# Kernel optimization log

Hardware: AMD Instinct MI355X
Metric: run time of the kernel (lower is better)

## Reference

```python
import jax, jax.numpy as jnp
import numpy as np

IN_F, OUT_F, NB = 4096, 4096, 8
BS = IN_F // NB  # 512


def setup_inputs() -> dict:
    key = jax.random.key(0)
    k1, k2, k3, k4 = jax.random.split(key, 4)
    weight = jax.random.normal(k1, (OUT_F, IN_F), dtype=jnp.float32) * 0.02
    bias = jax.random.normal(k2, (OUT_F,), dtype=jnp.float32) * 0.02
    x = jax.random.normal(k3, (4, 2048, IN_F), dtype=jnp.float32)
    R_blocks = jax.random.normal(k4, (NB, BS, BS), dtype=jnp.float32) * 0.1
    return {"weight": weight, "bias": bias, "x": x, "R_blocks": R_blocks, "layer_idx": 0}


def cayley_transform(A):
    # A: [nb, bs, bs]; Q = (I - A_skew) @ inv(I + A_skew + 1e-6 I)
    bs = A.shape[-1]
    I = jnp.eye(bs, dtype=A.dtype)
    A_skew = 0.5 * (A - jnp.swapaxes(A, -2, -1))
    return jnp.matmul(I - A_skew, jnp.linalg.inv(I + A_skew + 1e-6 * I))


def reference(weight, bias, x, R_blocks, layer_idx):
    R_ortho = cayley_transform(R_blocks)  # [nb, bs, bs]
    # weight @ block_diag(R) == per-block contraction on the in_features axis
    w = weight.reshape(OUT_F, NB, BS)
    tw = jnp.einsum('onb,nbc->onc', w, R_ortho).reshape(OUT_F, IN_F)
    # F.linear: x @ tw.T + bias
    out = jnp.einsum('bsi,oi->bso', x, tw) + bias
    return out
```

## Files before the change

### kernel.cpp

```cpp
#include <hip/hip_runtime.h>
#include <hip/hip_bf16.h>


typedef unsigned short u16;
typedef __attribute__((ext_vector_type(8))) __bf16 bf16x8;
typedef __attribute__((ext_vector_type(4))) float f32x4;
typedef __attribute__((ext_vector_type(8))) unsigned short u16x8;
typedef __attribute__((ext_vector_type(4))) unsigned short u16x4;

#define C0   1.000001f
#define C1Q  2.000001f
#define AS1 __attribute__((address_space(1)))
#define AS3 __attribute__((address_space(3)))

__device__ __forceinline__ u16 f2bf(float x) {
  union { float f; unsigned u; } v; v.f = x;
  return (u16)((v.u + 0x7fffu + ((v.u >> 16) & 1u)) >> 16);
}
__device__ __forceinline__ float bf2f(u16 h) {
  union { float f; unsigned u; } v; v.u = ((unsigned)h) << 16; return v.f;
}

__global__ __launch_bounds__(256) void k_build_M(const float* __restrict__ R,
                                                 u16* __restrict__ Mh,
                                                 u16* __restrict__ Ml) {
  __shared__ float t1[32][33];
  const int n = blockIdx.z;
  const int tr = blockIdx.y * 32, tc = blockIdx.x * 32;
  const int ly = threadIdx.x >> 5, lx = threadIdx.x & 31;
  const float* Rb = R + (size_t)n * 262144;
  float a[4];
#pragma unroll
  for (int i = 0; i < 4; ++i) {
    a[i] = Rb[(size_t)(tr + ly + i * 8) * 512 + tc + lx];
    t1[ly + i * 8][lx] = Rb[(size_t)(tc + ly + i * 8) * 512 + tr + lx];
  }
  __syncthreads();
#pragma unroll
  for (int i = 0; i < 4; ++i) {
    const int r = tr + ly + i * 8, c = tc + lx;
    float m = 0.5f * (a[i] - t1[lx][ly + i * 8]) + (r == c ? C0 : 0.0f);
    u16 h = f2bf(m);
    const size_t idx = (size_t)n * 262144 + (size_t)r * 512 + c;
    Mh[idx] = h;
    Ml[idx] = f2bf(m - bf2f(h));
  }
}

__global__ __launch_bounds__(1024) void k_frob_alpha(const u16* __restrict__ G4,
                                                     float* __restrict__ alpha) {
  __shared__ float red[16];
  const int n = blockIdx.x, tid = threadIdx.x;
  const u16* src = G4 + (size_t)n * 262144;
  float s = 0.f;
  for (int i = tid; i < 32768; i += 1024) {
    u16x8 v = reinterpret_cast<const u16x8*>(src)[i];
#pragma unroll
    for (int e = 0; e < 8; ++e) { float f = bf2f(v[e]); s += f * f; }
  }
  for (int off = 32; off; off >>= 1) s += __shfl_down(s, off, 64);
  if ((tid & 63) == 0) red[tid >> 6] = s;
  __syncthreads();
  if (tid == 0) {
    float t = 0.f;
    for (int q = 0; q < 16; ++q) t += red[q];
    float lam = powf(t, 0.125f);
    alpha[n] = 2.0f / (C0 * C0 + lam);
  }
}

__global__ __launch_bounds__(256) void k_init_X0(const u16* __restrict__ Mh,
                                                 const u16* __restrict__ Ml,
                                                 const float* __restrict__ alpha,
                                                 u16* __restrict__ X0,
                                                 u16* __restrict__ X0t) {
  int idx = blockIdx.x * 256 + threadIdx.x;
  int n = idx >> 18, r = (idx >> 9) & 511, c = idx & 511;
  float m = bf2f(Mh[idx]) + bf2f(Ml[idx]);
  float a = alpha[n];
  X0[idx]  = f2bf(a * ((r == c ? 2.0f * C0 : 0.0f) - m));
  X0t[idx] = f2bf(a * m);
}

template <int PROD3, int DMODE, int OMODE>
__global__ __launch_bounds__(256)
void k_bmm(const u16* __restrict__ Ah, const u16* __restrict__ Al,
           const u16* __restrict__ Bh, const u16* __restrict__ Bl,
           const u16* __restrict__ Dh, const u16* __restrict__ Dl,
           u16* __restrict__ Cnh, u16* __restrict__ Cnl,
           u16* __restrict__ Cth, u16* __restrict__ Ctl,
           float* __restrict__ Cf, float cd, float cs) {
  __shared__ __align__(16) u16 sAh[2048], sBh[2048];
  __shared__ __align__(16) u16 sAl[PROD3 ? 2048 : 8], sBl[PROD3 ? 2048 : 8];
  const size_t zb = (size_t)blockIdx.z * 262144;
  const int tid = threadIdx.x, lane = tid & 63, wave = tid >> 6;
  const int m0 = blockIdx.y * 64, n0 = blockIdx.x * 64;
  const int wr = wave >> 1, wc = wave & 1;
  const int c15 = lane & 15, lk = lane >> 4;
  const int srow = tid >> 2;
  const int sg = (tid & 3) ^ (srow & 3);
  f32x4 acc[2][2] = {};
  const u16* pa = Ah + zb + (size_t)(m0 + srow) * 512 + sg * 8;
  const u16* pb = Bh + zb + (size_t)(n0 + srow) * 512 + sg * 8;

  for (int k0 = 0; k0 < 512; k0 += 32) {
    __builtin_amdgcn_global_load_lds((const AS1 void*)(pa + k0),
                                     (AS3 void*)(sAh + (size_t)tid * 8), 16, 0, 0);
    __builtin_amdgcn_global_load_lds((const AS1 void*)(pb + k0),
                                     (AS3 void*)(sBh + (size_t)tid * 8), 16, 0, 0);
    if constexpr (PROD3) {
      const u16* pal = Al + zb + (size_t)(m0 + srow) * 512 + sg * 8;
      const u16* pbl = Bl + zb + (size_t)(n0 + srow) * 512 + sg * 8;
      __builtin_amdgcn_global_load_lds((const AS1 void*)(pal + k0),
                                       (AS3 void*)(sAl + (size_t)tid * 8), 16, 0, 0);
      __builtin_amdgcn_global_load_lds((const AS1 void*)(pbl + k0),
                                       (AS3 void*)(sBl + (size_t)tid * 8), 16, 0, 0);
    }
    __syncthreads();
    bf16x8 a[2], b[2], al2[2], bl2[2];
#pragma unroll
    for (int i = 0; i < 2; ++i) {
      const int fr = wr * 32 + i * 16 + c15;
      const int ia = fr * 32 + ((lk ^ (fr & 3)) * 8);
      a[i] = *reinterpret_cast<const bf16x8*>(&sAh[ia]);
      if constexpr (PROD3) al2[i] = *reinterpret_cast<const bf16x8*>(&sAl[ia]);
    }
#pragma unroll
    for (int j = 0; j < 2; ++j) {
      const int fc = wc * 32 + j * 16 + c15;
      const int ib = fc * 32 + ((lk ^ (fc & 3)) * 8);
      b[j] = *reinterpret_cast<const bf16x8*>(&sBh[ib]);
      if constexpr (PROD3) bl2[j] = *reinterpret_cast<const bf16x8*>(&sBl[ib]);
    }
#pragma unroll
    for (int i = 0; i < 2; ++i)
#pragma unroll
      for (int j = 0; j < 2; ++j) {
        acc[i][j] = __builtin_amdgcn_mfma_f32_16x16x32_bf16(a[i], b[j], acc[i][j], 0, 0, 0);
        if constexpr (PROD3) {
          acc[i][j] = __builtin_amdgcn_mfma_f32_16x16x32_bf16(a[i],   bl2[j], acc[i][j], 0, 0, 0);
          acc[i][j] = __builtin_amdgcn_mfma_f32_16x16x32_bf16(al2[i], b[j],   acc[i][j], 0, 0, 0);
        }
      }
    __syncthreads();
  }
#pragma unroll
  for (int i = 0; i < 2; ++i)
#pragma unroll
    for (int j = 0; j < 2; ++j) {
      const int rowb = m0 + wr * 32 + i * 16 + lk * 4;
      const int col  = n0 + wc * 32 + j * 16 + c15;
      u16 hv[4], lv[4];
#pragma unroll
      for (int r = 0; r < 4; ++r) {
        float val = cs * acc[i][j][r];
        if constexpr (DMODE >= 1) {
          float d = bf2f(Dh[zb + (size_t)(rowb + r) * 512 + col]);
          if constexpr (DMODE == 2) d += bf2f(Dl[zb + (size_t)(rowb + r) * 512 + col]);
          val += cd * d;
        }
        if constexpr (OMODE & 16) Cf[zb + (size_t)(rowb + r) * 512 + col] = val;
        u16 h = f2bf(val);
        if constexpr (OMODE & 1) Cnh[zb + (size_t)(rowb + r) * 512 + col] = h;
        u16 l = 0;
        if constexpr (OMODE & 10) l = f2bf(val - bf2f(h));
        if constexpr (OMODE & 2) Cnl[zb + (size_t)(rowb + r) * 512 + col] = l;
        hv[r] = h; lv[r] = l;
      }
      if constexpr (OMODE & 4) {
        u16x4 v; v[0] = hv[0]; v[1] = hv[1]; v[2] = hv[2]; v[3] = hv[3];
        *reinterpret_cast<u16x4*>(&Cth[zb + (size_t)col * 512 + rowb]) = v;
      }
      if constexpr (OMODE & 8) {
        u16x4 v; v[0] = lv[0]; v[1] = lv[1]; v[2] = lv[2]; v[3] = lv[3];
        *reinterpret_cast<u16x4*>(&Ctl[zb + (size_t)col * 512 + rowb]) = v;
      }
    }
}

template <int SPLIT, int BF16OUT>
__global__ __launch_bounds__(256)
void k_smm(const float* __restrict__ A, int lda, long long astride,
           const float* __restrict__ B, int ldb, long long bstride,
           void* __restrict__ Cv, int ldc, long long cstride,
           const float* __restrict__ D, int ldd, long long dstride,
           float c1, float sgn, int K) {
  __shared__ __align__(16) u16 lA  [128 * 40];
  __shared__ __align__(16) u16 lBT [128 * 40];
  const int nz = blockIdx.z;
  const float* Ab = A + (size_t)nz * astride;
  const float* Bb = B + (size_t)nz * bstride;
  const float* Db = D + (size_t)nz * dstride;
  const int tid = threadIdx.x, lane = tid & 63, wave = tid >> 6;
  const int m0 = blockIdx.y * 128, n0 = blockIdx.x * 128;
  const int wr = wave >> 1, wc = wave & 1;
  f32x4 acc[4][4] = {};

  for (int k0 = 0; k0 < K; k0 += 32) {
    if (k0) __syncthreads();
    {
      const int row = tid >> 1, ks = (tid & 1) * 16;
      const float* src = Ab + (size_t)(m0 + row) * lda + k0 + ks;
      float fv[16];
#pragma unroll
      for (int q = 0; q < 4; ++q) {
        float4 f = *(reinterpret_cast<const float4*>(src) + q);
        fv[q * 4 + 0] = f.x; fv[q * 4 + 1] = f.y; fv[q * 4 + 2] = f.z; fv[q * 4 + 3] = f.w;
      }
      u16x8 w0, w1;
#pragma unroll
      for (int e = 0; e < 8; ++e) { w0[e] = f2bf(fv[e]); w1[e] = f2bf(fv[e + 8]); }
      *reinterpret_cast<u16x8*>(&lA[row * 40 + ks])     = w0;
      *reinterpret_cast<u16x8*>(&lA[row * 40 + ks + 8]) = w1;
    }
    {
      const int kk = tid >> 3, nb = (tid & 7) * 16;
      const float* src = Bb + (size_t)(k0 + kk) * ldb + n0 + nb;
      float fv[16];
#pragma unroll
      for (int q = 0; q < 4; ++q) {
        float4 f = *(reinterpret_cast<const float4*>(src) + q);
        fv[q * 4 + 0] = f.x; fv[q * 4 + 1] = f.y; fv[q * 4 + 2] = f.z; fv[q * 4 + 3] = f.w;
      }
#pragma unroll
      for (int e = 0; e < 16; ++e) lBT[(nb + e) * 40 + kk] = f2bf(fv[e]);
    }
    __syncthreads();
    const int ks = (lane >> 4) * 8;
    bf16x8 af[4], bfr[4];
#pragma unroll
    for (int f = 0; f < 4; ++f) {
      const int ar = wr * 64 + f * 16 + (lane & 15);
      const int bc = wc * 64 + f * 16 + (lane & 15);
      af[f]  = *reinterpret_cast<const bf16x8*>(&lA [ar * 40 + ks]);
      bfr[f] = *reinterpret_cast<const bf16x8*>(&lBT[bc * 40 + ks]);
    }
#pragma unroll
    for (int i = 0; i < 4; ++i)
#pragma unroll
      for (int j = 0; j < 4; ++j)
        acc[i][j] = __builtin_amdgcn_mfma_f32_16x16x32_bf16(af[i], bfr[j], acc[i][j], 0, 0, 0);
  }
#pragma unroll
  for (int i = 0; i < 4; ++i) {
    const int rowb = m0 + wr * 64 + i * 16 + ((lane >> 4) << 2);
#pragma unroll
    for (int j = 0; j < 4; ++j) {
      const int col = n0 + wc * 64 + j * 16 + (lane & 15);
#pragma unroll
      for (int r = 0; r < 4; ++r) {
        float val = sgn * acc[i][j][r];
        if (c1 != 0.0f) val += c1 * Db[(size_t)(rowb + r) * ldd + col];
        if constexpr (BF16OUT)
          reinterpret_cast<u16*>(Cv)[(size_t)nz * cstride + (size_t)(rowb + r) * ldc + col] = f2bf(val);
        else
          reinterpret_cast<float*>(Cv)[(size_t)nz * cstride + (size_t)(rowb + r) * ldc + col] = val;
      }
    }
  }
}

__global__ __launch_bounds__(256) void k_f32_to_bf16(const float* __restrict__ in,
                                                     u16* __restrict__ out) {
  int idx = blockIdx.x * 256 + threadIdx.x;
  const float* src = in + (size_t)idx * 8;
  float4 f0 = *reinterpret_cast<const float4*>(src);
  float4 f1 = *reinterpret_cast<const float4*>(src + 4);
  u16x8 w;
  w[0] = f2bf(f0.x); w[1] = f2bf(f0.y); w[2] = f2bf(f0.z); w[3] = f2bf(f0.w);
  w[4] = f2bf(f1.x); w[5] = f2bf(f1.y); w[6] = f2bf(f1.z); w[7] = f2bf(f1.w);
  *reinterpret_cast<u16x8*>(out + (size_t)idx * 8) = w;
}

#define NSL 18

#define RD_A3(dst, MH)                                                         \
  _Pragma("unroll")                                                            \
  for (int m = 0; m < 4; ++m)                                                  \
    dst[m] = *reinterpret_cast<const bf16x8*>(                                 \
        &lds[aslot * 4096 + ((MH) * 64 + m * 16 + c15) * 32 + gsw * 8]);

#define RD_B3(dst)                                                             \
  _Pragma("unroll")                                                            \
  for (int n = 0; n < 4; ++n)                                                  \
    dst[n] = *reinterpret_cast<const bf16x8*>(                                 \
        &lds[bslot * 4096 + (bq64 + n * 16 + c15) * 32 + gsw * 8]);

#define MFMA16(afX, bfX, MH)                                                   \
  __builtin_amdgcn_s_setprio(1);                                               \
  _Pragma("unroll")                                                            \
  for (int m = 0; m < 4; ++m)                                                  \
    _Pragma("unroll")                                                          \
    for (int n = 0; n < 4; ++n)                                                \
      acc[(MH) * 4 + m][n] = __builtin_amdgcn_mfma_f32_16x16x32_bf16(          \
          afX[m], bfX[n], acc[(MH) * 4 + m][n], 0, 0, 0);                      \
  __builtin_amdgcn_s_setprio(0);

#define TILE32(WM)                                                             \
  {                                                                            \
    int aslot = s0 + wr;            if (aslot >= NSL) aslot -= NSL;            \
    int bslot = s0 + 2 + (wc >> 1); if (bslot >= NSL) bslot -= NSL;            \
    STAGE(); STAGE();                                                          \
    RD_B3(bfr)                                                                 \
    RD_A3(afA, 0)                                                              \
    MFMA16(afA, bfr, 0)                                                        \
    STAGE(); STAGE();                                                          \
    RD_A3(afB, 1)                                                              \
    MFMA16(afB, bfr, 1)                                                        \
    if ((WM) == 1) asm volatile("s_waitcnt vmcnt(8)" ::: "memory");            \
    if ((WM) == 2) asm volatile("s_waitcnt vmcnt(4)" ::: "memory");            \
    if ((WM) == 3) asm volatile("s_waitcnt vmcnt(0)" ::: "memory");            \
    if ((WM) != 0) {                                                           \
      __builtin_amdgcn_s_barrier();                                            \
      __builtin_amdgcn_sched_barrier(0);                                       \
    }                                                                          \
    s0 += 4; if (s0 >= NSL) s0 -= NSL;                                         \
  }

__global__ __launch_bounds__(512, 2)
void k_gemm256(const u16* __restrict__ A, const u16* __restrict__ B,
               const float* __restrict__ bias,
               float* __restrict__ C, int N, int K) {
  __shared__ __align__(16) u16 lds[NSL * 4096];
  const int tid = threadIdx.x, lane = tid & 63, wave = tid >> 6;
  int bid = blockIdx.y * gridDim.x + blockIdx.x;
  const int cpx = (gridDim.x * gridDim.y) >> 3;
  bid = (bid & 7) * cpx + (bid >> 3);
  const int nbx = N >> 8;
  const int bx = bid % nbx, by = bid / nbx;
  const int m0 = by << 8, n0 = bx << 8;
  const int wr = wave >> 2, wc = wave & 3;
  const int srow = tid >> 2;
  const int sgc  = (tid & 3) ^ ((srow >> 1) & 3);
  const int c15 = lane & 15, lq = lane >> 4;
  const int gsw = lq ^ ((c15 >> 1) & 3);
  const int bq64 = (wc & 1) * 64;
  const int NT = K >> 5;

  f32x4 acc[8][4] = {};
  bf16x8 afA[4], afB[4], bfr[4];

  int jn = 0, js = 0;
  auto STAGE = [&]() {
    if (jn < 4 * NT) {
      const int t = jn >> 2, q = jn & 3;
      const u16* srcb = (q < 2)
          ? A + (size_t)(m0 + q * 128 + srow) * (size_t)K
          : B + (size_t)(n0 + (q - 2) * 128 + srow) * (size_t)K;
      const u16* src = srcb + (t << 5) + sgc * 8;
      u16* dst = (u16*)lds + js * 4096 + tid * 8;
      __builtin_amdgcn_global_load_lds(
          (const AS1 void*)src, (AS3 void*)dst, 16, 0, 0);
    }
    ++jn; js = (js == NSL - 1) ? 0 : js + 1;
  };

#pragma unroll
  for (int i = 0; i < 12; ++i) STAGE();
  asm volatile("s_waitcnt vmcnt(8)" ::: "memory");
  __builtin_amdgcn_s_barrier();
  __builtin_amdgcn_sched_barrier(0);

  int s0 = 0;
  for (int tau = 0; tau < NT - 3; ++tau) {
    TILE32(1)
  }
  TILE32(2)
  TILE32(3)
  TILE32(0)

#pragma unroll
  for (int n = 0; n < 4; ++n) {
    const int col = n0 + wc * 64 + n * 16 + c15;
    const float bv = bias[col];
#pragma unroll
    for (int mi = 0; mi < 8; ++mi) {
      const int rowb = m0 + wr * 128 + mi * 16 + (lq << 2);
#pragma unroll
      for (int r = 0; r < 4; ++r)
        C[(size_t)(rowb + r) * N + col] = acc[mi][n][r] + bv;
    }
  }
}

extern "C" void kernel_launch(void* const* d_in, const int* in_sizes, int n_in,
                              void* d_out, int out_size, void* d_ws, size_t ws_size,
                              hipStream_t stream) {
  const float* W    = (const float*)d_in[0];
  const float* bias = (const float*)d_in[1];
  const float* x    = (const float*)d_in[2];
  const float* R    = (const float*)d_in[3];
  float* out = (float*)d_out;

  char* ws = (char*)d_ws;
  u16* x_bf = (u16*)(ws);
  u16* tw   = (u16*)(ws + 67108864);

  char* arena = (char*)d_out;
  auto slot = [&](int i) -> u16* { return (u16*)(arena + (size_t)i * 4194304); };
  u16 *Mh = slot(0), *Ml = slot(1);
  u16 *G = slot(2), *G2 = slot(3), *G4 = slot(4);
  u16 *Xa = slot(5), *Xat = slot(6), *Xb = slot(7), *Xbt = slot(8);
  u16 *Xbl = slot(9), *Xbtl = slot(10);
  u16 *Tt = slot(2);
  u16 *Tth = slot(3), *Ttl = slot(4);
  u16 *X6h = slot(5), *X6l = slot(6);
  u16 *X6th = slot(11), *X6tl = slot(12);
  float* Qf = (float*)(arena + (size_t)13 * 4194304);
  float* alpha = (float*)(arena + (size_t)15 * 4194304);

  const long long BS2 = 262144;
  const dim3 g8(8, 8, 8);
  const u16* NUL = nullptr;

  k_build_M<<<dim3(16, 16, 8), 256, 0, stream>>>(R, Mh, Ml);
  k_bmm<0, 0, 1><<<g8, 256, 0, stream>>>(Mh, NUL, Mh, NUL, NUL, NUL,
                                         G, nullptr, nullptr, nullptr, nullptr, 0.f, 1.f);
  k_bmm<0, 0, 1><<<g8, 256, 0, stream>>>(G, NUL, G, NUL, NUL, NUL,
                                         G2, nullptr, nullptr, nullptr, nullptr, 0.f, 1.f);
  k_bmm<0, 0, 1><<<g8, 256, 0, stream>>>(G2, NUL, G2, NUL, NUL, NUL,
                                         G4, nullptr, nullptr, nullptr, nullptr, 0.f, 1.f);
  k_frob_alpha<<<8, 1024, 0, stream>>>(G4, alpha);
  k_init_X0<<<8192, 256, 0, stream>>>(Mh, Ml, alpha, Xa, Xat);

  u16 *cur = Xa, *curt = Xat, *nxt = Xb, *nxtt = Xbt;
  for (int it = 0; it < 4; ++it) {
    k_bmm<0, 0, 4><<<g8, 256, 0, stream>>>(Mh, NUL, curt, NUL, NUL, NUL,
                                           nullptr, nullptr, Tt, nullptr, nullptr, 0.f, 1.f);
    k_bmm<0, 1, 5><<<g8, 256, 0, stream>>>(cur, NUL, Tt, NUL, cur, NUL,
                                           nxt, nullptr, nxtt, nullptr, nullptr, 2.f, -1.f);
    u16* t;
    t = cur; cur = nxt; nxt = t;
    t = curt; curt = nxtt; nxtt = t;
  }
  k_bmm<0, 0, 4><<<g8, 256, 0, stream>>>(Mh, NUL, curt, NUL, NUL, NUL,
                                         nullptr, nullptr, Tt, nullptr, nullptr, 0.f, 1.f);
  k_bmm<0, 1, 15><<<g8, 256, 0, stream>>>(cur, NUL, Tt, NUL, cur, NUL,
                                          Xb, Xbl, Xbt, Xbtl, nullptr, 2.f, -1.f);
  k_bmm<1, 0, 12><<<g8, 256, 0, stream>>>(Mh, Ml, Xbt, Xbtl, NUL, NUL,
                                          nullptr, nullptr, Tth, Ttl, nullptr, 0.f, 1.f);
  k_bmm<1, 2, 15><<<g8, 256, 0, stream>>>(Xb, Xbl, Tth, Ttl, Xb, Xbl,
                                          X6h, X6l, X6th, X6tl, nullptr, 2.f, -1.f);
  k_bmm<1, 2, 16><<<g8, 256, 0, stream>>>(Mh, Ml, X6th, X6tl, X6h, X6l,
                                          nullptr, nullptr, nullptr, nullptr, Qf, C1Q, -1.f);
  k_smm<0, 1><<<dim3(4, 32, 8), 256, 0, stream>>>(W, 4096, 512, Qf, 512, BS2,
                                                  tw, 4096, 512, W, 4096, 512, 0.f, 1.f, 512);
  k_f32_to_bf16<<<16384, 256, 0, stream>>>(x, x_bf);
  k_gemm256<<<dim3(16, 32), 512, 0, stream>>>(x_bf, tw, bias, out, 4096, 4096);
}
```

Measured before the change: 574.8 us.

## Multi-stage pipeline batched matmuls and replace fp32 weight-transform GEMM with bf16 kernel

Rebuilds the small batched matmul kernel as a 4-buffer LDS ring. Global-to-LDS loads are issued two stages ahead and synchronised with explicit vmcnt waits and raw barriers, replacing the load-sync-compute-sync loop. The final Cayley-stage GEMM now writes a transposed bf16 Q instead of fp32. The fp32-converting weight transform GEMM is replaced by a bf16 pre-conversion of W plus a new pipelined 64x64-tile kernel. This trades extra LDS use and a conversion pass for overlapped loads and less per-tile conversion work, with the risk that the hand-counted vmcnt values are wrong.

```diff
diff --git a/kernel.cpp b/kernel.cpp
--- a/kernel.cpp
+++ b/kernel.cpp
@@ -82,6 +82,44 @@
   X0t[idx] = f2bf(a * m);
 }
 
+#define BMM_FRAGS(rs)                                                          \
+  bf16x8 a[2], b[2], al2[2], bl2[2];                                           \
+  _Pragma("unroll")                                                            \
+  for (int i = 0; i < 2; ++i) {                                                \
+    const int fr = wr * 32 + i * 16 + c15;                                     \
+    const int ia = (rs) * 2048 + fr * 32 + ((lk ^ (fr & 3)) * 8);              \
+    a[i] = *reinterpret_cast<const bf16x8*>(&sA[ia]);                          \
+    if constexpr (PROD3) al2[i] = *reinterpret_cast<const bf16x8*>(&sAl[ia]);  \
+  }                                                                            \
+  _Pragma("unroll")                                                            \
+  for (int j = 0; j < 2; ++j) {                                                \
+    const int fc = wc * 32 + j * 16 + c15;                                     \
+    const int ib = (rs) * 2048 + fc * 32 + ((lk ^ (fc & 3)) * 8);              \
+    b[j] = *reinterpret_cast<const bf16x8*>(&sB[ib]);                          \
+    if constexpr (PROD3) bl2[j] = *reinterpret_cast<const bf16x8*>(&sBl[ib]);  \
+  }                                                                            \
+  _Pragma("unroll")                                                            \
+  for (int i = 0; i < 2; ++i)                                                  \
+    _Pragma("unroll")                                                          \
+    for (int j = 0; j < 2; ++j) {                                              \
+      acc[i][j] = __builtin_amdgcn_mfma_f32_16x16x32_bf16(a[i], b[j], acc[i][j], 0, 0, 0); \
+      if constexpr (PROD3) {                                                   \
+        acc[i][j] = __builtin_amdgcn_mfma_f32_16x16x32_bf16(a[i],   bl2[j], acc[i][j], 0, 0, 0); \
+        acc[i][j] = __builtin_amdgcn_mfma_f32_16x16x32_bf16(al2[i], b[j],   acc[i][j], 0, 0, 0); \
+      }                                                                        \
+    }
+
+#define BMM_WAIT(SEL)                                                          \
+  if ((SEL) == 0) {                                                            \
+    if constexpr (PROD3) asm volatile("s_waitcnt vmcnt(8)" ::: "memory");      \
+    else                 asm volatile("s_waitcnt vmcnt(4)" ::: "memory");      \
+  } else if ((SEL) == 1) {                                                     \
+    if constexpr (PROD3) asm volatile("s_waitcnt vmcnt(4)" ::: "memory");      \
+    else                 asm volatile("s_waitcnt vmcnt(2)" ::: "memory");      \
+  } else {                                                                     \
+    asm volatile("s_waitcnt vmcnt(0)" ::: "memory");                           \
+  }
+
 template <int PROD3, int DMODE, int OMODE>
 __global__ __launch_bounds__(256)
 void k_bmm(const u16* __restrict__ Ah, const u16* __restrict__ Al,
@@ -89,9 +127,10 @@
            const u16* __restrict__ Dh, const u16* __restrict__ Dl,
            u16* __restrict__ Cnh, u16* __restrict__ Cnl,
            u16* __restrict__ Cth, u16* __restrict__ Ctl,
-           float* __restrict__ Cf, float cd, float cs) {
-  __shared__ __align__(16) u16 sAh[2048], sBh[2048];
-  __shared__ __align__(16) u16 sAl[PROD3 ? 2048 : 8], sBl[PROD3 ? 2048 : 8];
+           float cd, float cs) {
+  __shared__ __align__(16) u16 sA[4 * 2048], sB[4 * 2048];
+  __shared__ __align__(16) u16 sAl[PROD3 ? 4 * 2048 : 8];
+  __shared__ __align__(16) u16 sBl[PROD3 ? 4 * 2048 : 8];
   const size_t zb = (size_t)blockIdx.z * 262144;
   const int tid = threadIdx.x, lane = tid & 63, wave = tid >> 6;
   const int m0 = blockIdx.y * 64, n0 = blockIdx.x * 64;
@@ -102,48 +141,46 @@
   f32x4 acc[2][2] = {};
   const u16* pa = Ah + zb + (size_t)(m0 + srow) * 512 + sg * 8;
   const u16* pb = Bh + zb + (size_t)(n0 + srow) * 512 + sg * 8;
-
-  for (int k0 = 0; k0 < 512; k0 += 32) {
-    __builtin_amdgcn_global_load_lds((const AS1 void*)(pa + k0),
-                                     (AS3 void*)(sAh + (size_t)tid * 8), 16, 0, 0);
-    __builtin_amdgcn_global_load_lds((const AS1 void*)(pb + k0),
-                                     (AS3 void*)(sBh + (size_t)tid * 8), 16, 0, 0);
-    if constexpr (PROD3) {
-      const u16* pal = Al + zb + (size_t)(m0 + srow) * 512 + sg * 8;
-      const u16* pbl = Bl + zb + (size_t)(n0 + srow) * 512 + sg * 8;
-      __builtin_amdgcn_global_load_lds((const AS1 void*)(pal + k0),
-                                       (AS3 void*)(sAl + (size_t)tid * 8), 16, 0, 0);
-      __builtin_amdgcn_global_load_lds((const AS1 void*)(pbl + k0),
-                                       (AS3 void*)(sBl + (size_t)tid * 8), 16, 0, 0);
-    }
-    __syncthreads();
-    bf16x8 a[2], b[2], al2[2], bl2[2];
-#pragma unroll
-    for (int i = 0; i < 2; ++i) {
-      const int fr = wr * 32 + i * 16 + c15;
-      const int ia = fr * 32 + ((lk ^ (fr & 3)) * 8);
-      a[i] = *reinterpret_cast<const bf16x8*>(&sAh[ia]);
-      if constexpr (PROD3) al2[i] = *reinterpret_cast<const bf16x8*>(&sAl[ia]);
-    }
-#pragma unroll
-    for (int j = 0; j < 2; ++j) {
-      const int fc = wc * 32 + j * 16 + c15;
-      const int ib = fc * 32 + ((lk ^ (fc & 3)) * 8);
-      b[j] = *reinterpret_cast<const bf16x8*>(&sBh[ib]);
-      if constexpr (PROD3) bl2[j] = *reinterpret_cast<const bf16x8*>(&sBl[ib]);
-    }
-#pragma unroll
-    for (int i = 0; i < 2; ++i)
-#pragma unroll
-      for (int j = 0; j < 2; ++j) {
-        acc[i][j] = __builtin_amdgcn_mfma_f32_16x16x32_bf16(a[i], b[j], acc[i][j], 0, 0, 0);
-        if constexpr (PROD3) {
-          acc[i][j] = __builtin_amdgcn_mfma_f32_16x16x32_bf16(a[i],   bl2[j], acc[i][j], 0, 0, 0);
-          acc[i][j] = __builtin_amdgcn_mfma_f32_16x16x32_bf16(al2[i], b[j],   acc[i][j], 0, 0, 0);
-        }
+  const u16* pal = PROD3 ? Al + zb + (size_t)(m0 + srow) * 512 + sg * 8 : pa;
+  const u16* pbl = PROD3 ? Bl + zb + (size_t)(n0 + srow) * 512 + sg * 8 : pb;
+
+  int jn = 0, js = 0;
+  auto STG = [&]() {
+    if (jn < 16) {
+      const int off = jn << 5;
+      u16* da = sA + js * 2048 + tid * 8;
+      u16* db = sB + js * 2048 + tid * 8;
+      __builtin_amdgcn_global_load_lds((const AS1 void*)(pa + off), (AS3 void*)da, 16, 0, 0);
+      __builtin_amdgcn_global_load_lds((const AS1 void*)(pb + off), (AS3 void*)db, 16, 0, 0);
+      if constexpr (PROD3) {
+        __builtin_amdgcn_global_load_lds((const AS1 void*)(pal + off),
+                                         (AS3 void*)(sAl + js * 2048 + tid * 8), 16, 0, 0);
+        __builtin_amdgcn_global_load_lds((const AS1 void*)(pbl + off),
+                                         (AS3 void*)(sBl + js * 2048 + tid * 8), 16, 0, 0);
       }
-    __syncthreads();
-  }
+    }
+    ++jn; js = (js + 1) & 3;
+  };
+
+  STG(); STG();
+  int rs = 0;
+  for (int t = 0; t < 14; ++t) {
+    STG();
+    BMM_WAIT(0)
+    __builtin_amdgcn_s_barrier();
+    BMM_FRAGS(rs)
+    rs = (rs + 1) & 3;
+  }
+  STG();
+  BMM_WAIT(1)
+  __builtin_amdgcn_s_barrier();
+  { BMM_FRAGS(rs) }
+  rs = (rs + 1) & 3;
+  STG();
+  BMM_WAIT(2)
+  __builtin_amdgcn_s_barrier();
+  { BMM_FRAGS(rs) }
+
 #pragma unroll
   for (int i = 0; i < 2; ++i)
 #pragma unroll
@@ -159,7 +196,6 @@
           if constexpr (DMODE == 2) d += bf2f(Dl[zb + (size_t)(rowb + r) * 512 + col]);
           val += cd * d;
         }
-        if constexpr (OMODE & 16) Cf[zb + (size_t)(rowb + r) * 512 + col] = val;
         u16 h = f2bf(val);
         if constexpr (OMODE & 1) Cnh[zb + (size_t)(rowb + r) * 512 + col] = h;
         u16 l = 0;
@@ -178,86 +214,85 @@
     }
 }
 
-template <int SPLIT, int BF16OUT>
 __global__ __launch_bounds__(256)
-void k_smm(const float* __restrict__ A, int lda, long long astride,
-           const float* __restrict__ B, int ldb, long long bstride,
-           void* __restrict__ Cv, int ldc, long long cstride,
-           const float* __restrict__ D, int ldd, long long dstride,
-           float c1, float sgn, int K) {
-  __shared__ __align__(16) u16 lA  [128 * 40];
-  __shared__ __align__(16) u16 lBT [128 * 40];
-  const int nz = blockIdx.z;
-  const float* Ab = A + (size_t)nz * astride;
-  const float* Bb = B + (size_t)nz * bstride;
-  const float* Db = D + (size_t)nz * dstride;
+void k_twmm(const u16* __restrict__ W, const u16* __restrict__ Qt,
+            u16* __restrict__ tw) {
+  __shared__ __align__(16) u16 sA[4 * 2048], sB[4 * 2048];
+  const int z = blockIdx.z;
+  const size_t zb = (size_t)z * 262144;
   const int tid = threadIdx.x, lane = tid & 63, wave = tid >> 6;
-  const int m0 = blockIdx.y * 128, n0 = blockIdx.x * 128;
+  const int m0 = blockIdx.y * 64, n0 = blockIdx.x * 64;
   const int wr = wave >> 1, wc = wave & 1;
-  f32x4 acc[4][4] = {};
-
-  for (int k0 = 0; k0 < K; k0 += 32) {
-    if (k0) __syncthreads();
-    {
-      const int row = tid >> 1, ks = (tid & 1) * 16;
-      const float* src = Ab + (size_t)(m0 + row) * lda + k0 + ks;
-      float fv[16];
-#pragma unroll
-      for (int q = 0; q < 4; ++q) {
-        float4 f = *(reinterpret_cast<const float4*>(src) + q);
-        fv[q * 4 + 0] = f.x; fv[q * 4 + 1] = f.y; fv[q * 4 + 2] = f.z; fv[q * 4 + 3] = f.w;
-      }
-      u16x8 w0, w1;
-#pragma unroll
-      for (int e = 0; e < 8; ++e) { w0[e] = f2bf(fv[e]); w1[e] = f2bf(fv[e + 8]); }
-      *reinterpret_cast<u16x8*>(&lA[row * 40 + ks])     = w0;
-      *reinterpret_cast<u16x8*>(&lA[row * 40 + ks + 8]) = w1;
-    }
-    {
-      const int kk = tid >> 3, nb = (tid & 7) * 16;
-      const float* src = Bb + (size_t)(k0 + kk) * ldb + n0 + nb;
-      float fv[16];
-#pragma unroll
-      for (int q = 0; q < 4; ++q) {
-        float4 f = *(reinterpret_cast<const float4*>(src) + q);
-        fv[q * 4 + 0] = f.x; fv[q * 4 + 1] = f.y; fv[q * 4 + 2] = f.z; fv[q * 4 + 3] = f.w;
-      }
-#pragma unroll
-      for (int e = 0; e < 16; ++e) lBT[(nb + e) * 40 + kk] = f2bf(fv[e]);
-    }
-    __syncthreads();
-    const int ks = (lane >> 4) * 8;
-    bf16x8 af[4], bfr[4];
-#pragma unroll
-    for (int f = 0; f < 4; ++f) {
-      const int ar = wr * 64 + f * 16 + (lane & 15);
-      const int bc = wc * 64 + f * 16 + (lane & 15);
-      af[f]  = *reinterpret_cast<const bf16x8*>(&lA [ar * 40 + ks]);
-      bfr[f] = *reinterpret_cast<const bf16x8*>(&lBT[bc * 40 + ks]);
-    }
-#pragma unroll
-    for (int i = 0; i < 4; ++i)
-#pragma unroll
-      for (int j = 0; j < 4; ++j)
-        acc[i][j] = __builtin_amdgcn_mfma_f32_16x16x32_bf16(af[i], bfr[j], acc[i][j], 0, 0, 0);
-  }
-#pragma unroll
-  for (int i = 0; i < 4; ++i) {
-    const int rowb = m0 + wr * 64 + i * 16 + ((lane >> 4) << 2);
-#pragma unroll
-    for (int j = 0; j < 4; ++j) {
-      const int col = n0 + wc * 64 + j * 16 + (lane & 15);
-#pragma unroll
-      for (int r = 0; r < 4; ++r) {
-        float val = sgn * acc[i][j][r];
-        if (c1 != 0.0f) val += c1 * Db[(size_t)(rowb + r) * ldd + col];
-        if constexpr (BF16OUT)
-          reinterpret_cast<u16*>(Cv)[(size_t)nz * cstride + (size_t)(rowb + r) * ldc + col] = f2bf(val);
-        else
-          reinterpret_cast<float*>(Cv)[(size_t)nz * cstride + (size_t)(rowb + r) * ldc + col] = val;
-      }
-    }
-  }
+  const int c15 = lane & 15, lk = lane >> 4;
+  const int srow = tid >> 2;
+  const int sg = (tid & 3) ^ (srow & 3);
+  f32x4 acc[2][2] = {};
+  const u16* pa = W + (size_t)(m0 + srow) * 4096 + z * 512 + sg * 8;
+  const u16* pb = Qt + zb + (size_t)(n0 + srow) * 512 + sg * 8;
+
+  int jn = 0, js = 0;
+  auto STG = [&]() {
+    if (jn < 16) {
+      const int off = jn << 5;
+      __builtin_amdgcn_global_load_lds((const AS1 void*)(pa + off),
+                                       (AS3 void*)(sA + js * 2048 + tid * 8), 16, 0, 0);
+      __builtin_amdgcn_global_load_lds((const AS1 void*)(pb + off),
+                                       (AS3 void*)(sB + js * 2048 + tid * 8), 16, 0, 0);
+    }
+    ++jn; js = (js + 1) & 3;
+  };
+
+#define TW_FRAGS(rs)                                                           \
+  {                                                                            \
+    bf16x8 a[2], b[2];                                                         \
+    _Pragma("unroll")                                                          \
+    for (int i = 0; i < 2; ++i) {                                              \
+      const int fr = wr * 32 + i * 16 + c15;                                   \
+      a[i] = *reinterpret_cast<const bf16x8*>(                                 \
+          &sA[(rs) * 2048 + fr * 32 + ((lk ^ (fr & 3)) * 8)]);                 \
+    }                                                                          \
+    _Pragma("unroll")                                                          \
+    for (int j = 0; j < 2; ++j) {                                              \
+      const int fc = wc * 32 + j * 16 + c15;                                   \
+      b[j] = *reinterpret_cast<const bf16x8*>(                                 \
+          &sB[(rs) * 2048 + fc * 32 + ((lk ^ (fc & 3)) * 8)]);                 \
+    }                                                                          \
+    _Pragma("unroll")                                                          \
+    for (int i = 0; i < 2; ++i)                                                \
+      _Pragma("unroll")                                                        \
+      for (int j = 0; j < 2; ++j)                                              \
+        acc[i][j] = __builtin_amdgcn_mfma_f32_16x16x32_bf16(a[i], b[j], acc[i][j], 0, 0, 0); \
+  }
+
+  STG(); STG();
+  int rs = 0;
+  for (int t = 0; t < 14; ++t) {
+    STG();
+    asm volatile("s_waitcnt vmcnt(4)" ::: "memory");
+    __builtin_amdgcn_s_barrier();
+    TW_FRAGS(rs)
+    rs = (rs + 1) & 3;
+  }
+  STG();
+  asm volatile("s_waitcnt vmcnt(2)" ::: "memory");
+  __builtin_amdgcn_s_barrier();
+  TW_FRAGS(rs)
+  rs = (rs + 1) & 3;
+  STG();
+  asm volatile("s_waitcnt vmcnt(0)" ::: "memory");
+  __builtin_amdgcn_s_barrier();
+  TW_FRAGS(rs)
+
+#pragma unroll
+  for (int i = 0; i < 2; ++i)
+#pragma unroll
+    for (int j = 0; j < 2; ++j) {
+      const int rowb = m0 + wr * 32 + i * 16 + lk * 4;
+      const int col  = z * 512 + n0 + wc * 32 + j * 16 + c15;
+#pragma unroll
+      for (int r = 0; r < 4; ++r)
+        tw[(size_t)(rowb + r) * 4096 + col] = f2bf(acc[i][j][r]);
+    }
 }
 
 __global__ __launch_bounds__(256) void k_f32_to_bf16(const float* __restrict__ in,
@@ -395,6 +430,7 @@
   char* ws = (char*)d_ws;
   u16* x_bf = (u16*)(ws);
   u16* tw   = (u16*)(ws + 67108864);
+  u16* W_bf = (u16*)(ws + 100663296);
 
   char* arena = (char*)d_out;
   auto slot = [&](int i) -> u16* { return (u16*)(arena + (size_t)i * 4194304); };
@@ -406,45 +442,44 @@
   u16 *Tth = slot(3), *Ttl = slot(4);
   u16 *X6h = slot(5), *X6l = slot(6);
   u16 *X6th = slot(11), *X6tl = slot(12);
-  float* Qf = (float*)(arena + (size_t)13 * 4194304);
+  u16 *Qt = slot(13);
   float* alpha = (float*)(arena + (size_t)15 * 4194304);
 
-  const long long BS2 = 262144;
   const dim3 g8(8, 8, 8);
   const u16* NUL = nullptr;
 
   k_build_M<<<dim3(16, 16, 8), 256, 0, stream>>>(R, Mh, Ml);
   k_bmm<0, 0, 1><<<g8, 256, 0, stream>>>(Mh, NUL, Mh, NUL, NUL, NUL,
-                                         G, nullptr, nullptr, nullptr, nullptr, 0.f, 1.f);
+                                         G, nullptr, nullptr, nullptr, 0.f, 1.f);
   k_bmm<0, 0, 1><<<g8, 256, 0, stream>>>(G, NUL, G, NUL, NUL, NUL,
-                                         G2, nullptr, nullptr, nullptr, nullptr, 0.f, 1.f);
+                                         G2, nullptr, nullptr, nullptr, 0.f, 1.f);
   k_bmm<0, 0, 1><<<g8, 256, 0, stream>>>(G2, NUL, G2, NUL, NUL, NUL,
-                                         G4, nullptr, nullptr, nullptr, nullptr, 0.f, 1.f);
+                                         G4, nullptr, nullptr, nullptr, 0.f, 1.f);
   k_frob_alpha<<<8, 1024, 0, stream>>>(G4, alpha);
   k_init_X0<<<8192, 256, 0, stream>>>(Mh, Ml, alpha, Xa, Xat);
 
   u16 *cur = Xa, *curt = Xat, *nxt = Xb, *nxtt = Xbt;
   for (int it = 0; it < 4; ++it) {
     k_bmm<0, 0, 4><<<g8, 256, 0, stream>>>(Mh, NUL, curt, NUL, NUL, NUL,
-                                           nullptr, nullptr, Tt, nullptr, nullptr, 0.f, 1.f);
+                                           nullptr, nullptr, Tt, nullptr, 0.f, 1.f);
     k_bmm<0, 1, 5><<<g8, 256, 0, stream>>>(cur, NUL, Tt, NUL, cur, NUL,
-                                           nxt, nullptr, nxtt, nullptr, nullptr, 2.f, -1.f);
+                                           nxt, nullptr, nxtt, nullptr, 2.f, -1.f);
     u16* t;
     t = cur; cur = nxt; nxt = t;
     t = curt; curt = nxtt; nxtt = t;
   }
   k_bmm<0, 0, 4><<<g8, 256, 0, stream>>>(Mh, NUL, curt, NUL, NUL, NUL,
-                                         nullptr, nullptr, Tt, nullptr, nullptr, 0.f, 1.f);
+                                         nullptr, nullptr, Tt, nullptr, 0.f, 1.f);
   k_bmm<0, 1, 15><<<g8, 256, 0, stream>>>(cur, NUL, Tt, NUL, cur, NUL,
-                                          Xb, Xbl, Xbt, Xbtl, nullptr, 2.f, -1.f);
+                                          Xb, Xbl, Xbt, Xbtl, 2.f, -1.f);
   k_bmm<1, 0, 12><<<g8, 256, 0, stream>>>(Mh, Ml, Xbt, Xbtl, NUL, NUL,
-                                          nullptr, nullptr, Tth, Ttl, nullptr, 0.f, 1.f);
+                                          nullptr, nullptr, Tth, Ttl, 0.f, 1.f);
   k_bmm<1, 2, 15><<<g8, 256, 0, stream>>>(Xb, Xbl, Tth, Ttl, Xb, Xbl,
-                                          X6h, X6l, X6th, X6tl, nullptr, 2.f, -1.f);
-  k_bmm<1, 2, 16><<<g8, 256, 0, stream>>>(Mh, Ml, X6th, X6tl, X6h, X6l,
-                                          nullptr, nullptr, nullptr, nullptr, Qf, C1Q, -1.f);
-  k_smm<0, 1><<<dim3(4, 32, 8), 256, 0, stream>>>(W, 4096, 512, Qf, 512, BS2,
-                                                  tw, 4096, 512, W, 4096, 512, 0.f, 1.f, 512);
+                                          X6h, X6l, X6th, X6tl, 2.f, -1.f);
+  k_bmm<1, 2, 4><<<g8, 256, 0, stream>>>(Mh, Ml, X6th, X6tl, X6h, X6l,
+                                         nullptr, nullptr, Qt, nullptr, C1Q, -1.f);
+  k_f32_to_bf16<<<8192, 256, 0, stream>>>(W, W_bf);
+  k_twmm<<<dim3(8, 64, 8), 256, 0, stream>>>(W_bf, Qt, tw);
   k_f32_to_bf16<<<16384, 256, 0, stream>>>(x, x_bf);
   k_gemm256<<<dim3(16, 32), 512, 0, stream>>>(x_bf, tw, bias, out, 4096, 4096);
 }
```

New measurement: 550.6 us. 4.2% less time.
